# Optimization experiments

Hardware: AMD Instinct MI355X
Metric: run time of the kernel (lower is better)

The kernel has to match this reference:

```python
import jax, jax.numpy as jnp
import numpy as np

B, S, D, H = 2, 2048, 1024, 16
DK = D // H
ROPE_BASE = 10000.0


def setup_inputs() -> dict:
    key = jax.random.key(0)
    ks = jax.random.split(key, 6)
    x = jax.random.normal(ks[0], (B, S, D), dtype=jnp.float32)
    # causal mask, broadcastable to [B,H,S,S]; masked_fill where mask==0
    mask = jnp.tril(jnp.ones((S, S), dtype=bool))[None, None]
    position_ids = jnp.tile(jnp.arange(S, dtype=jnp.int32)[None, :], (B, 1))
    sc = 1.0 / np.sqrt(D)
    Wq = jax.random.normal(ks[1], (D, D), dtype=jnp.float32) * sc
    Wk = jax.random.normal(ks[2], (D, D), dtype=jnp.float32) * sc
    Wv = jax.random.normal(ks[3], (D, D), dtype=jnp.float32) * sc
    Wo = jax.random.normal(ks[4], (D, D), dtype=jnp.float32) * sc
    bo = jnp.zeros((D,), dtype=jnp.float32)
    return {"x": x, "mask": mask, "position_ids": position_ids,
            "Wq": Wq, "Wk": Wk, "Wv": Wv, "Wo": Wo, "bo": bo}


def _rotate_half(t):
    t1, t2 = t[..., : t.shape[-1] // 2], t[..., t.shape[-1] // 2:]
    return jnp.concatenate((-t2, t1), axis=-1)


def reference(x, mask, position_ids, Wq, Wk, Wv, Wo, bo):
    b, s, d = x.shape
    h, dk = H, DK
    scale = 1.0 / np.sqrt(dk)

    def proj(W):  # torch Linear: x @ W.T -> [b,h,s,dk]
        return (x @ W.T).reshape(b, s, h, dk).transpose(0, 2, 1, 3)

    Q, K, V = proj(Wq), proj(Wk), proj(Wv)

    # rotary tables (computed in fp32, matching RotaryEmbedding)
    inv_freq = 1.0 / (ROPE_BASE ** (jnp.arange(0, dk, 2, dtype=jnp.float32) / dk))
    t = jnp.arange(s, dtype=jnp.float32)
    freqs = jnp.outer(t, inv_freq)            # [s, dk/2]
    emb = jnp.concatenate((freqs, freqs), -1) # [s, dk]
    cos = jnp.cos(emb)[position_ids][:, None]  # [b,1,s,dk]
    sin = jnp.sin(emb)[position_ids][:, None]
    Q = Q * cos + _rotate_half(Q) * sin
    K = K * cos + _rotate_half(K) * sin

    scores = jnp.einsum('bhqd,bhkd->bhqk', Q, K) * scale
    scores = jnp.where(mask, scores, jnp.float32(-1e9))
    attn = jax.nn.softmax(scores, axis=-1)  # dropout is identity in eval
    out = jnp.einsum('bhqk,bhkd->bhqd', attn, V)
    out = out.transpose(0, 2, 1, 3).reshape(b, s, d)
    return out @ Wo.T + bo
```

## Files before the change

### kernel.cpp

```cpp
#include <hip/hip_runtime.h>
#include <hip/hip_bf16.h>
#include <cstdint>

#define BB 2
#define SS 2048
#define DD 1024
#define HH 16
#define DK 64
#define MROWS (BB*SS)
#define NQKV  (3*DD)

typedef __bf16 bf16x8 __attribute__((ext_vector_type(8)));
typedef float  f32x4  __attribute__((ext_vector_type(4)));
typedef float  f32x16 __attribute__((ext_vector_type(16)));
typedef unsigned u32x2 __attribute__((ext_vector_type(2)));

static __device__ __forceinline__ unsigned short f2bf(float f) {
    __bf16 h = (__bf16)f;
    return __builtin_bit_cast(unsigned short, h);
}
static __device__ __forceinline__ float bf2f(unsigned short u) {
    return (float)__builtin_bit_cast(__bf16, u);
}

#define GLOAD16(gsrc, ldst) \
    __builtin_amdgcn_global_load_lds((const __attribute__((address_space(1))) void*)(gsrc), \
                                     (__attribute__((address_space(3))) void*)(ldst), 16, 0, 0)

static __device__ __forceinline__ void pl32_swap(unsigned &x, unsigned &y) {
#if __has_builtin(__builtin_amdgcn_permlane32_swap)
    u32x2 r = __builtin_amdgcn_permlane32_swap(x, y, false, false);
    x = r[0]; y = r[1];
#else
    asm volatile("v_permlane32_swap_b32 %0, %1" : "+v"(x), "+v"(y));
#endif
}
static __device__ __forceinline__ float swap_half(float v, bool hi) {
    unsigned x = __builtin_bit_cast(unsigned, v), y = x;
    pl32_swap(x, y);
    return __builtin_bit_cast(float, hi ? x : y);
}
template<int BASE> static __device__ __forceinline__ bf16x8 cvt_chunk(const f32x16 &p) {
    unsigned x0, y0, x1, y1;
    asm("v_cvt_pk_bf16_f32 %0, %1, %2" : "=v"(x0) : "v"(p[BASE+0]), "v"(p[BASE+1]));
    asm("v_cvt_pk_bf16_f32 %0, %1, %2" : "=v"(y0) : "v"(p[BASE+4]), "v"(p[BASE+5]));
    asm("v_cvt_pk_bf16_f32 %0, %1, %2" : "=v"(x1) : "v"(p[BASE+2]), "v"(p[BASE+3]));
    asm("v_cvt_pk_bf16_f32 %0, %1, %2" : "=v"(y1) : "v"(p[BASE+6]), "v"(p[BASE+7]));
    pl32_swap(x0, y0);
    pl32_swap(x1, y1);
    union { unsigned u[4]; bf16x8 v; } r;
    r.u[0] = x0; r.u[1] = x1; r.u[2] = y0; r.u[3] = y1;
    return r.v;
}

__global__ void cast_all(const float* __restrict__ x,  const float* __restrict__ wq,
                         const float* __restrict__ wk, const float* __restrict__ wv,
                         const float* __restrict__ wo,
                         unsigned short* __restrict__ xb, unsigned short* __restrict__ wqkv,
                         unsigned short* __restrict__ wob)
{
    const int NX = MROWS * DD;
    const int NW = DD * DD;
    const int total = (NX + 4 * NW) / 8;
    for (int i = blockIdx.x * blockDim.x + threadIdx.x; i < total; i += gridDim.x * blockDim.x) {
        int base = i * 8;
        const float* src; unsigned short* dst; int off;
        if      (base < NX)          { src = x;  dst = xb;          off = base; }
        else if (base < NX + NW)     { src = wq; dst = wqkv;        off = base - NX; }
        else if (base < NX + 2*NW)   { src = wk; dst = wqkv + NW;   off = base - NX - NW; }
        else if (base < NX + 3*NW)   { src = wv; dst = wqkv + 2*NW; off = base - NX - 2*NW; }
        else                         { src = wo; dst = wob;         off = base - NX - 3*NW; }
        float4 a = *(const float4*)(src + off);
        float4 b = *(const float4*)(src + off + 4);
        union { unsigned short s[8]; uint4 v; } u;
        u.s[0] = f2bf(a.x); u.s[1] = f2bf(a.y); u.s[2] = f2bf(a.z); u.s[3] = f2bf(a.w);
        u.s[4] = f2bf(b.x); u.s[5] = f2bf(b.y); u.s[6] = f2bf(b.z); u.s[7] = f2bf(b.w);
        *(uint4*)(dst + off) = u.v;
    }
}

__global__ void rope_table(float* __restrict__ tabc, float* __restrict__ tabs)
{
    int i = blockIdx.x * blockDim.x + threadIdx.x;
    int s = i >> 5, d = i & 31;
    float inv = exp2f(-(float)d * (13.287712379549449f / 32.f));
    float ang = (float)s * inv;
    tabc[i] = cosf(ang);
    tabs[i] = sinf(ang);
}

__global__ __launch_bounds__(256) void gemm_qkv(
    const unsigned short* __restrict__ A, const unsigned short* __restrict__ Bm,
    const int* __restrict__ pids,
    const float* __restrict__ tabc, const float* __restrict__ tabs,
    unsigned short* __restrict__ Qb, unsigned short* __restrict__ Kb,
    unsigned short* __restrict__ Vr)
{
    __shared__ __align__(16) unsigned short sA[128 * 64];
    __shared__ __align__(16) unsigned short sB[128 * 64];
    const int tid = threadIdx.x;
    const int w = tid >> 6, l = tid & 63;
    const int wm = w >> 1, wn = w & 1;
    const int lr = l & 15, lg = l >> 4;
    const int swz = (blockIdx.x & 7) * 96 + (blockIdx.x >> 3);
    const int bx = swz % 24, by = swz / 24;
    const int mBase = by * 128, nBase = bx * 128;
    const int srow = tid >> 3;
    const int skof = (tid & 7) * 8;

    f32x4 acc[4][4] = {};

    for (int kt = 0; kt < DD; kt += 64) {
        __syncthreads();
        #pragma unroll
        for (int i = 0; i < 4; ++i) {
            const unsigned short* srcA = A + (size_t)(mBase + i*32 + srow) * DD + kt + skof;
            GLOAD16(srcA, &sA[i*2048 + w*512]);
            const unsigned short* srcB = Bm + (size_t)(nBase + i*32 + srow) * DD + kt + skof;
            GLOAD16(srcB, &sB[i*2048 + w*512]);
        }
        __syncthreads();
        #pragma unroll
        for (int kk = 0; kk < 2; ++kk) {
            bf16x8 af[4], bfv[4];
            #pragma unroll
            for (int mi = 0; mi < 4; ++mi)
                af[mi] = *(const bf16x8*)&sA[(wm*64 + mi*16 + lr)*64 + kk*32 + lg*8];
            #pragma unroll
            for (int ni = 0; ni < 4; ++ni)
                bfv[ni] = *(const bf16x8*)&sB[(wn*64 + ni*16 + lr)*64 + kk*32 + lg*8];
            #pragma unroll
            for (int mi = 0; mi < 4; ++mi)
                #pragma unroll
                for (int ni = 0; ni < 4; ++ni)
                    acc[mi][ni] = __builtin_amdgcn_mfma_f32_16x16x32_bf16(af[mi], bfv[ni], acc[mi][ni], 0, 0, 0);
        }
    }

    if (bx < 16) {
        const bool isQ = bx < 8;
        unsigned short* dst = isQ ? Qb : Kb;
        const float qsc = isQ ? 0.1803368801111244f : 1.0f;
        const int colbase = (bx & 7)*128 + wn*64;
        #pragma unroll
        for (int mi = 0; mi < 4; ++mi) {
            #pragma unroll
            for (int j = 0; j < 4; ++j) {
                int row = mBase + wm*64 + mi*16 + lg*4 + j;
                int pos = pids[row];
                #pragma unroll
                for (int ni = 0; ni < 2; ++ni) {
                    int d = ni*16 + lr;
                    float cc = tabc[pos*32 + d];
                    float sn = tabs[pos*32 + d];
                    float a  = acc[mi][ni][j];
                    float bb = acc[mi][ni+2][j];
                    dst[(size_t)row * DD + colbase + d]      = f2bf((a*cc - bb*sn) * qsc);
                    dst[(size_t)row * DD + colbase + d + 32] = f2bf((bb*cc + a*sn) * qsc);
                }
            }
        }
    } else {
        const int colbase = (bx - 16)*128 + wn*64;
        #pragma unroll
        for (int mi = 0; mi < 4; ++mi) {
            #pragma unroll
            for (int j = 0; j < 4; ++j) {
                int row = mBase + wm*64 + mi*16 + lg*4 + j;
                #pragma unroll
                for (int ni = 0; ni < 4; ++ni)
                    Vr[(size_t)row * DD + colbase + ni*16 + lr] = f2bf(acc[mi][ni][j]);
            }
        }
    }
}

__global__ __launch_bounds__(256) void gemm_bt(
    const unsigned short* __restrict__ A, const unsigned short* __restrict__ Bm,
    float* __restrict__ Cout, const float* __restrict__ bias,
    int M, int N, int K)
{
    __shared__ __align__(16) unsigned short sA[128 * 64];
    __shared__ __align__(16) unsigned short sB[128 * 64];
    const int tid = threadIdx.x;
    const int w = tid >> 6, l = tid & 63;
    const int wm = w >> 1, wn = w & 1;
    const int lr = l & 15, lg = l >> 4;
    const int nwg = gridDim.x;
    const int cpx = nwg >> 3;
    const int swz = (blockIdx.x & 7) * cpx + (blockIdx.x >> 3);
    const int nbx = N >> 7;
    const int bx = swz % nbx, by = swz / nbx;
    const int mBase = by * 128, nBase = bx * 128;
    const int srow = tid >> 3;
    const int skof = (tid & 7) * 8;

    f32x4 acc[4][4] = {};

    for (int kt = 0; kt < K; kt += 64) {
        __syncthreads();
        #pragma unroll
        for (int i = 0; i < 4; ++i) {
            const unsigned short* srcA = A + (size_t)(mBase + i*32 + srow) * K + kt + skof;
            GLOAD16(srcA, &sA[i*2048 + w*512]);
            const unsigned short* srcB = Bm + (size_t)(nBase + i*32 + srow) * K + kt + skof;
            GLOAD16(srcB, &sB[i*2048 + w*512]);
        }
        __syncthreads();
        #pragma unroll
        for (int kk = 0; kk < 2; ++kk) {
            bf16x8 af[4], bfv[4];
            #pragma unroll
            for (int mi = 0; mi < 4; ++mi)
                af[mi] = *(const bf16x8*)&sA[(wm*64 + mi*16 + lr)*64 + kk*32 + lg*8];
            #pragma unroll
            for (int ni = 0; ni < 4; ++ni)
                bfv[ni] = *(const bf16x8*)&sB[(wn*64 + ni*16 + lr)*64 + kk*32 + lg*8];
            #pragma unroll
            for (int mi = 0; mi < 4; ++mi)
                #pragma unroll
                for (int ni = 0; ni < 4; ++ni)
                    acc[mi][ni] = __builtin_amdgcn_mfma_f32_16x16x32_bf16(af[mi], bfv[ni], acc[mi][ni], 0, 0, 0);
        }
    }
    #pragma unroll
    for (int mi = 0; mi < 4; ++mi) {
        #pragma unroll
        for (int j = 0; j < 4; ++j) {
            int row = mBase + wm*64 + mi*16 + lg*4 + j;
            #pragma unroll
            for (int ni = 0; ni < 4; ++ni) {
                int col = nBase + wn*64 + ni*16 + lr;
                Cout[(size_t)row * N + col] = acc[mi][ni][j] + bias[col];
            }
        }
    }
}

__global__ __launch_bounds__(256) void v_transpose(
    const unsigned short* __restrict__ Vr, unsigned short* __restrict__ Vt)
{
    __shared__ __align__(16) unsigned short sT[64 * 64];
    const int bh = blockIdx.y;
    const int st = blockIdx.x;
    const int b = bh >> 4, h = bh & 15;
    const int tid = threadIdx.x;
    #pragma unroll
    for (int i = 0; i < 2; ++i) {
        int c = tid + i*256;
        int s = c >> 3, cb = c & 7;
        const unsigned short* src = Vr + (size_t)(b*SS + st*64 + s) * DD + h*64 + cb*8;
        uint4 v = *(const uint4*)src;
        *(uint4*)&sT[s*64 + ((cb ^ (s >> 3)) * 8)] = v;
    }
    __syncthreads();
    #pragma unroll
    for (int i = 0; i < 2; ++i) {
        int c = tid + i*256;
        int d = c >> 3, sb = c & 7;
        union { unsigned short u[8]; uint4 v; } o;
        #pragma unroll
        for (int e = 0; e < 8; ++e) {
            int s = sb*8 + e;
            o.u[e] = sT[s*64 + (((d >> 3) ^ (s >> 3)) * 8) + (d & 7)];
        }
        *(uint4*)(Vt + (size_t)(bh*64 + d) * SS + st*64 + sb*8) = o.v;
    }
}

__global__ __launch_bounds__(128, 2) void attn_fwd(
    const unsigned short* __restrict__ Qb,
    const unsigned short* __restrict__ Kb,
    const unsigned short* __restrict__ Vt,
    unsigned short* __restrict__ Ob)
{
    __shared__ __align__(16) unsigned short sK[2][64 * 64];
    __shared__ __align__(16) unsigned short sV[2][64 * 64];
    const int tid = threadIdx.x;
    const int w = tid >> 6, l = tid & 63;
    const int lq = l & 31;
    const int hi5 = l >> 5;
    const bool hb = hi5 != 0;

    const int xcd = blockIdx.x & 7;
    const int c   = blockIdx.x >> 3;
    const int g   = c >> 5;
    const int s_  = c & 31;
    const int qt  = (g & 1) ? (31 - s_) : s_;
    const int bh  = xcd * 4 + g;
    const int b = bh >> 4, h = bh & 15;

    const int srow2 = tid >> 3;
    const int skof  = (tid & 7) * 8;
    const int sksw  = skof ^ ((srow2 & 7) * 8);
    const int sw    = (lq & 7) * 8;
    const float THR = 12.0f;

    const unsigned kR = (unsigned)((b*SS + srow2) * DD + h*64 + sksw);
    const unsigned vR = (unsigned)((bh*64 + srow2) * SS + sksw);

    bf16x8 qf[4];
    {
        const unsigned short* qp = Qb + (size_t)(b*SS + qt*64 + w*32 + lq) * DD + h*64 + hi5*8;
        #pragma unroll
        for (int dkc = 0; dkc < 4; ++dkc)
            qf[dkc] = *(const bf16x8*)(qp + dkc*16);
    }
    const int q_lane = qt*64 + w*32 + lq;

    f32x16 o0 = {}, o1 = {};
    float mrow = -3.0e38f, lsum = 0.f;
    int cur = 0;

    #pragma unroll
    for (int i = 0; i < 4; ++i) {
        GLOAD16(Kb + kR + (unsigned)(i << 14), &sK[0][i*1024 + w*512]);
        GLOAD16(Vt + vR + (unsigned)(i << 15), &sV[0][i*1024 + w*512]);
    }

    for (int kt = 0; kt <= qt; ++kt) {
        __syncthreads();
        if (kt < qt) {
            unsigned ko = (unsigned)(kt + 1) << 16;
            unsigned vo = (unsigned)(kt + 1) << 6;
            #pragma unroll
            for (int i = 0; i < 4; ++i) {
                GLOAD16(Kb + kR + ko + (unsigned)(i << 14), &sK[cur^1][i*1024 + w*512]);
                GLOAD16(Vt + vR + vo + (unsigned)(i << 15), &sV[cur^1][i*1024 + w*512]);
            }
        }

        f32x16 p0 = {}, p1 = {};
        __builtin_amdgcn_s_setprio(1);
        #pragma unroll
        for (int dkc = 0; dkc < 4; ++dkc) {
            bf16x8 k0 = *(const bf16x8*)&sK[cur][lq*64 + ((dkc*16 + hi5*8) ^ sw)];
            p0 = __builtin_amdgcn_mfma_f32_32x32x16_bf16(k0, qf[dkc], p0, 0, 0, 0);
        }
        #pragma unroll
        for (int dkc = 0; dkc < 4; ++dkc) {
            bf16x8 k1 = *(const bf16x8*)&sK[cur][(32 + lq)*64 + ((dkc*16 + hi5*8) ^ sw)];
            p1 = __builtin_amdgcn_mfma_f32_32x32x16_bf16(k1, qf[dkc], p1, 0, 0, 0);
        }
        __builtin_amdgcn_s_setprio(0);

        if (kt == qt) {
            const int kb0 = kt*64 + 4*hi5;
            #pragma unroll
            for (int r = 0; r < 16; ++r) {
                const int cr = (r & 3) + 8*(r >> 2);
                if (kb0 + cr > q_lane)      p0[r] = -1e30f;
                if (kb0 + 32 + cr > q_lane) p1[r] = -1e30f;
            }
        }

        float tt[16];
        #pragma unroll
        for (int r = 0; r < 16; ++r) tt[r] = fmaxf(p0[r], p1[r]);
        #pragma unroll
        for (int s2 = 8; s2 >= 1; s2 >>= 1)
            #pragma unroll
            for (int r = 0; r < 8; ++r)
                if (r < s2) tt[r] = fmaxf(tt[r], tt[r + s2]);
        float tmx = fmaxf(tt[0], swap_half(tt[0], hb));

        float growth = tmx - mrow;
        if (!__all(growth <= THR)) {
            float mnew = fmaxf(mrow, tmx);
            float alpha = exp2f(mrow - mnew);
            lsum *= alpha;
            mrow = mnew;
            #pragma unroll
            for (int r = 0; r < 16; ++r) { o0[r] *= alpha; o1[r] *= alpha; }
        }

        #pragma unroll
        for (int r = 0; r < 16; ++r) {
            p0[r] = exp2f(p0[r] - mrow);
            p1[r] = exp2f(p1[r] - mrow);
        }
        float st[16];
        #pragma unroll
        for (int r = 0; r < 16; ++r) st[r] = p0[r] + p1[r];
        #pragma unroll
        for (int s2 = 8; s2 >= 1; s2 >>= 1)
            #pragma unroll
            for (int r = 0; r < 8; ++r)
                if (r < s2) st[r] += st[r + s2];
        lsum += st[0];

        __builtin_amdgcn_s_setprio(1);
        {
            bf16x8 pa, vf;
            pa = cvt_chunk<0>(p0);
            vf = *(const bf16x8*)&sV[cur][lq*64 + ((0*16 + hi5*8) ^ sw)];
            o0 = __builtin_amdgcn_mfma_f32_32x32x16_bf16(vf, pa, o0, 0, 0, 0);
            vf = *(const bf16x8*)&sV[cur][(32 + lq)*64 + ((0*16 + hi5*8) ^ sw)];
            o1 = __builtin_amdgcn_mfma_f32_32x32x16_bf16(vf, pa, o1, 0, 0, 0);
            pa = cvt_chunk<8>(p0);
            vf = *(const bf16x8*)&sV[cur][lq*64 + ((1*16 + hi5*8) ^ sw)];
            o0 = __builtin_amdgcn_mfma_f32_32x32x16_bf16(vf, pa, o0, 0, 0, 0);
            vf = *(const bf16x8*)&sV[cur][(32 + lq)*64 + ((1*16 + hi5*8) ^ sw)];
            o1 = __builtin_amdgcn_mfma_f32_32x32x16_bf16(vf, pa, o1, 0, 0, 0);
            pa = cvt_chunk<0>(p1);
            vf = *(const bf16x8*)&sV[cur][lq*64 + ((2*16 + hi5*8) ^ sw)];
            o0 = __builtin_amdgcn_mfma_f32_32x32x16_bf16(vf, pa, o0, 0, 0, 0);
            vf = *(const bf16x8*)&sV[cur][(32 + lq)*64 + ((2*16 + hi5*8) ^ sw)];
            o1 = __builtin_amdgcn_mfma_f32_32x32x16_bf16(vf, pa, o1, 0, 0, 0);
            pa = cvt_chunk<8>(p1);
            vf = *(const bf16x8*)&sV[cur][lq*64 + ((3*16 + hi5*8) ^ sw)];
            o0 = __builtin_amdgcn_mfma_f32_32x32x16_bf16(vf, pa, o0, 0, 0, 0);
            vf = *(const bf16x8*)&sV[cur][(32 + lq)*64 + ((3*16 + hi5*8) ^ sw)];
            o1 = __builtin_amdgcn_mfma_f32_32x32x16_bf16(vf, pa, o1, 0, 0, 0);
        }
        __builtin_amdgcn_s_setprio(0);
        cur ^= 1;
    }

    __syncthreads();
    float ls = lsum + swap_half(lsum, hb);
    float inv = 1.f / ls;
    unsigned short* sO = &sK[0][0] + w * 2048;

    #pragma unroll
    for (int g2 = 0; g2 < 4; ++g2) {
        unsigned ua, ub; uint2 t2;
        float v0 = o0[g2*4+0]*inv, v1 = o0[g2*4+1]*inv, v2 = o0[g2*4+2]*inv, v3 = o0[g2*4+3]*inv;
        asm("v_cvt_pk_bf16_f32 %0, %1, %2" : "=v"(ua) : "v"(v0), "v"(v1));
        asm("v_cvt_pk_bf16_f32 %0, %1, %2" : "=v"(ub) : "v"(v2), "v"(v3));
        t2.x = ua; t2.y = ub;
        *(uint2*)&sO[lq*64 + g2*8 + hi5*4] = t2;
        float w0 = o1[g2*4+0]*inv, w1 = o1[g2*4+1]*inv, w2 = o1[g2*4+2]*inv, w3 = o1[g2*4+3]*inv;
        asm("v_cvt_pk_bf16_f32 %0, %1, %2" : "=v"(ua) : "v"(w0), "v"(w1));
        asm("v_cvt_pk_bf16_f32 %0, %1, %2" : "=v"(ub) : "v"(w2), "v"(w3));
        t2.x = ua; t2.y = ub;
        *(uint2*)&sO[lq*64 + 32 + g2*8 + hi5*4] = t2;
    }
    asm volatile("s_waitcnt lgkmcnt(0)" ::: "memory");
    __builtin_amdgcn_sched_barrier(0);

    const int row = l >> 1, cb2 = (l & 1) * 32;
    const unsigned short* sOr = sO + row*64 + cb2;
    unsigned short* gp = Ob + (size_t)(b*SS + qt*64 + w*32 + row) * DD + h*64 + cb2;
    #pragma unroll
    for (int c2 = 0; c2 < 4; ++c2)
        *(uint4*)(gp + c2*8) = *(const uint4*)(sOr + c2*8);
}

extern "C" void kernel_launch(void* const* d_in, const int* in_sizes, int n_in,
                              void* d_out, int out_size, void* d_ws, size_t ws_size,
                              hipStream_t stream)
{
    const float* x  = (const float*)d_in[0];
    const int* pids = (const int*)d_in[2];
    const float* wq = (const float*)d_in[3];
    const float* wk = (const float*)d_in[4];
    const float* wv = (const float*)d_in[5];
    const float* wo = (const float*)d_in[6];
    const float* bo = (const float*)d_in[7];
    float* out = (float*)d_out;

    char* ws = (char*)d_ws;
    unsigned short* xb   = (unsigned short*)(ws);
    unsigned short* wqkv = (unsigned short*)(ws + (size_t)( 8u<<20));
    unsigned short* wob  = (unsigned short*)(ws + (size_t)(14u<<20));
    unsigned short* Vr   = (unsigned short*)(ws + (size_t)(16u<<20));
    unsigned short* Qb   = (unsigned short*)(ws + (size_t)(40u<<20));
    unsigned short* Kb   = (unsigned short*)(ws + (size_t)(48u<<20));
    unsigned short* Vt   = (unsigned short*)(ws + (size_t)(56u<<20));
    float* tabc          = (float*)(ws + (size_t)(64u<<20));
    float* tabs          = (float*)(ws + (size_t)(64u<<20) + (256u<<10));
    unsigned short* Ob   = xb;

    cast_all<<<dim3(4096), dim3(256), 0, stream>>>(x, wq, wk, wv, wo, xb, wqkv, wob);
    rope_table<<<dim3(256), dim3(256), 0, stream>>>(tabc, tabs);
    gemm_qkv<<<dim3(768), dim3(256), 0, stream>>>(
        xb, wqkv, pids, tabc, tabs, Qb, Kb, Vr);
    v_transpose<<<dim3(32, 32), dim3(256), 0, stream>>>(Vr, Vt);
    attn_fwd<<<dim3(1024), dim3(128), 0, stream>>>(Qb, Kb, Vt, Ob);
    gemm_bt<<<dim3(256), dim3(256), 0, stream>>>(
        Ob, wob, out, bo, MROWS, DD, DD);
}
```

Baseline: 151.5 us.

## Double-buffer shared memory tiles in QKV and output GEMMs

Both bf16 MFMA GEMM kernels now keep two shared-memory buffers for the A and B tiles. A prologue loads the first K-tile, and each iteration issues the next tile's global-to-LDS loads before computing on the current one. This removes one barrier per iteration and lets memory traffic overlap the MFMA work. In exchange, shared memory per block doubles to 64 KB, which can lower occupancy. Correctness relies on the barrier at the top of each iteration also waiting for the outstanding async loads.

```diff
diff --git a/kernel.cpp b/kernel.cpp
--- a/kernel.cpp
+++ b/kernel.cpp
@@ -96,8 +96,8 @@
     unsigned short* __restrict__ Qb, unsigned short* __restrict__ Kb,
     unsigned short* __restrict__ Vr)
 {
-    __shared__ __align__(16) unsigned short sA[128 * 64];
-    __shared__ __align__(16) unsigned short sB[128 * 64];
+    __shared__ __align__(16) unsigned short sA[2][128 * 64];
+    __shared__ __align__(16) unsigned short sB[2][128 * 64];
     const int tid = threadIdx.x;
     const int w = tid >> 6, l = tid & 63;
     const int wm = w >> 1, wn = w & 1;
@@ -110,31 +110,38 @@
 
     f32x4 acc[4][4] = {};
 
+    #pragma unroll
+    for (int i = 0; i < 4; ++i) {
+        GLOAD16(A  + (size_t)(mBase + i*32 + srow) * DD + skof, &sA[0][i*2048 + w*512]);
+        GLOAD16(Bm + (size_t)(nBase + i*32 + srow) * DD + skof, &sB[0][i*2048 + w*512]);
+    }
+    int cur = 0;
+
     for (int kt = 0; kt < DD; kt += 64) {
         __syncthreads();
-        #pragma unroll
-        for (int i = 0; i < 4; ++i) {
-            const unsigned short* srcA = A + (size_t)(mBase + i*32 + srow) * DD + kt + skof;
-            GLOAD16(srcA, &sA[i*2048 + w*512]);
-            const unsigned short* srcB = Bm + (size_t)(nBase + i*32 + srow) * DD + kt + skof;
-            GLOAD16(srcB, &sB[i*2048 + w*512]);
-        }
-        __syncthreads();
+        if (kt + 64 < DD) {
+            #pragma unroll
+            for (int i = 0; i < 4; ++i) {
+                GLOAD16(A  + (size_t)(mBase + i*32 + srow) * DD + kt + 64 + skof, &sA[cur^1][i*2048 + w*512]);
+                GLOAD16(Bm + (size_t)(nBase + i*32 + srow) * DD + kt + 64 + skof, &sB[cur^1][i*2048 + w*512]);
+            }
+        }
         #pragma unroll
         for (int kk = 0; kk < 2; ++kk) {
             bf16x8 af[4], bfv[4];
             #pragma unroll
             for (int mi = 0; mi < 4; ++mi)
-                af[mi] = *(const bf16x8*)&sA[(wm*64 + mi*16 + lr)*64 + kk*32 + lg*8];
+                af[mi] = *(const bf16x8*)&sA[cur][(wm*64 + mi*16 + lr)*64 + kk*32 + lg*8];
             #pragma unroll
             for (int ni = 0; ni < 4; ++ni)
-                bfv[ni] = *(const bf16x8*)&sB[(wn*64 + ni*16 + lr)*64 + kk*32 + lg*8];
+                bfv[ni] = *(const bf16x8*)&sB[cur][(wn*64 + ni*16 + lr)*64 + kk*32 + lg*8];
             #pragma unroll
             for (int mi = 0; mi < 4; ++mi)
                 #pragma unroll
                 for (int ni = 0; ni < 4; ++ni)
                     acc[mi][ni] = __builtin_amdgcn_mfma_f32_16x16x32_bf16(af[mi], bfv[ni], acc[mi][ni], 0, 0, 0);
         }
+        cur ^= 1;
     }
 
     if (bx < 16) {
@@ -180,8 +187,8 @@
     float* __restrict__ Cout, const float* __restrict__ bias,
     int M, int N, int K)
 {
-    __shared__ __align__(16) unsigned short sA[128 * 64];
-    __shared__ __align__(16) unsigned short sB[128 * 64];
+    __shared__ __align__(16) unsigned short sA[2][128 * 64];
+    __shared__ __align__(16) unsigned short sB[2][128 * 64];
     const int tid = threadIdx.x;
     const int w = tid >> 6, l = tid & 63;
     const int wm = w >> 1, wn = w & 1;
@@ -197,31 +204,38 @@
 
     f32x4 acc[4][4] = {};
 
+    #pragma unroll
+    for (int i = 0; i < 4; ++i) {
+        GLOAD16(A  + (size_t)(mBase + i*32 + srow) * K + skof, &sA[0][i*2048 + w*512]);
+        GLOAD16(Bm + (size_t)(nBase + i*32 + srow) * K + skof, &sB[0][i*2048 + w*512]);
+    }
+    int cur = 0;
+
     for (int kt = 0; kt < K; kt += 64) {
         __syncthreads();
-        #pragma unroll
-        for (int i = 0; i < 4; ++i) {
-            const unsigned short* srcA = A + (size_t)(mBase + i*32 + srow) * K + kt + skof;
-            GLOAD16(srcA, &sA[i*2048 + w*512]);
-            const unsigned short* srcB = Bm + (size_t)(nBase + i*32 + srow) * K + kt + skof;
-            GLOAD16(srcB, &sB[i*2048 + w*512]);
-        }
-        __syncthreads();
+        if (kt + 64 < K) {
+            #pragma unroll
+            for (int i = 0; i < 4; ++i) {
+                GLOAD16(A  + (size_t)(mBase + i*32 + srow) * K + kt + 64 + skof, &sA[cur^1][i*2048 + w*512]);
+                GLOAD16(Bm + (size_t)(nBase + i*32 + srow) * K + kt + 64 + skof, &sB[cur^1][i*2048 + w*512]);
+            }
+        }
         #pragma unroll
         for (int kk = 0; kk < 2; ++kk) {
             bf16x8 af[4], bfv[4];
             #pragma unroll
             for (int mi = 0; mi < 4; ++mi)
-                af[mi] = *(const bf16x8*)&sA[(wm*64 + mi*16 + lr)*64 + kk*32 + lg*8];
+                af[mi] = *(const bf16x8*)&sA[cur][(wm*64 + mi*16 + lr)*64 + kk*32 + lg*8];
             #pragma unroll
             for (int ni = 0; ni < 4; ++ni)
-                bfv[ni] = *(const bf16x8*)&sB[(wn*64 + ni*16 + lr)*64 + kk*32 + lg*8];
+                bfv[ni] = *(const bf16x8*)&sB[cur][(wn*64 + ni*16 + lr)*64 + kk*32 + lg*8];
             #pragma unroll
             for (int mi = 0; mi < 4; ++mi)
                 #pragma unroll
                 for (int ni = 0; ni < 4; ++ni)
                     acc[mi][ni] = __builtin_amdgcn_mfma_f32_16x16x32_bf16(af[mi], bfv[ni], acc[mi][ni], 0, 0, 0);
         }
+        cur ^= 1;
     }
     #pragma unroll
     for (int mi = 0; mi < 4; ++mi) {
```

New measurement: 147.4 us. -2.7%, faster.

## Share K/V tiles across four waves covering 128 query rows per block

Applied to the files above, without the earlier changes.

The attention kernel grows from 2 to 4 waves per block, so each block covers 128 query rows instead of 64 and each staged K/V tile is reused by twice as many queries. This halves the grid and the global-to-LDS K/V traffic per query. The block-to-tile mapping is redone to pair short and long causal tiles, and the causal mask is now tested per wave. In exchange, lower-row waves do some wasted work on fully masked tiles near the diagonal, and fewer, larger blocks may balance less evenly across CUs.

```diff
diff --git a/kernel.cpp b/kernel.cpp
--- a/kernel.cpp
+++ b/kernel.cpp
@@ -268,7 +268,7 @@
     }
 }
 
-__global__ __launch_bounds__(128, 2) void attn_fwd(
+__global__ __launch_bounds__(256, 2) void attn_fwd(
     const unsigned short* __restrict__ Qb,
     const unsigned short* __restrict__ Kb,
     const unsigned short* __restrict__ Vt,
@@ -282,52 +282,54 @@
     const int hi5 = l >> 5;
     const bool hb = hi5 != 0;
 
-    const int xcd = blockIdx.x & 7;
-    const int c   = blockIdx.x >> 3;
-    const int g   = c >> 5;
-    const int s_  = c & 31;
-    const int qt  = (g & 1) ? (31 - s_) : s_;
-    const int bh  = xcd * 4 + g;
+    const int xcd  = blockIdx.x & 7;
+    const int c    = blockIdx.x >> 3;
+    const int gsel = c & 3;
+    const int t    = c >> 2;
+    const int qt   = (t < 8) ? t : 23 - t;
+    const int bh   = xcd * 4 + gsel;
     const int b = bh >> 4, h = bh & 15;
 
-    const int srow2 = tid >> 3;
-    const int skof  = (tid & 7) * 8;
-    const int sksw  = skof ^ ((srow2 & 7) * 8);
-    const int sw    = (lq & 7) * 8;
+    const int srow = tid >> 3;
+    const int skof = (tid & 7) * 8;
+    const int sksw = skof ^ ((srow & 7) * 8);
+    const int sw   = (lq & 7) * 8;
     const float THR = 12.0f;
 
-    const unsigned kR = (unsigned)((b*SS + srow2) * DD + h*64 + sksw);
-    const unsigned vR = (unsigned)((bh*64 + srow2) * SS + sksw);
+    const unsigned kR0 = (unsigned)((b*SS + srow) * DD + h*64 + sksw);
+    const unsigned kR1 = kR0 + (unsigned)(32 * DD);
+    const unsigned vR0 = (unsigned)((bh*64 + srow) * SS + sksw);
+    const unsigned vR1 = vR0 + (unsigned)(32 * SS);
 
     bf16x8 qf[4];
     {
-        const unsigned short* qp = Qb + (size_t)(b*SS + qt*64 + w*32 + lq) * DD + h*64 + hi5*8;
+        const unsigned short* qp = Qb + (size_t)(b*SS + qt*128 + w*32 + lq) * DD + h*64 + hi5*8;
         #pragma unroll
         for (int dkc = 0; dkc < 4; ++dkc)
             qf[dkc] = *(const bf16x8*)(qp + dkc*16);
     }
-    const int q_lane = qt*64 + w*32 + lq;
+    const int q_lane = qt*128 + w*32 + lq;
+    const int wbase  = qt*128 + w*32;
+    const int total  = 2*qt + 2;
 
     f32x16 o0 = {}, o1 = {};
     float mrow = -3.0e38f, lsum = 0.f;
     int cur = 0;
 
-    #pragma unroll
-    for (int i = 0; i < 4; ++i) {
-        GLOAD16(Kb + kR + (unsigned)(i << 14), &sK[0][i*1024 + w*512]);
-        GLOAD16(Vt + vR + (unsigned)(i << 15), &sV[0][i*1024 + w*512]);
-    }
-
-    for (int kt = 0; kt <= qt; ++kt) {
+    GLOAD16(Kb + kR0, &sK[0][w*512]);
+    GLOAD16(Kb + kR1, &sK[0][2048 + w*512]);
+    GLOAD16(Vt + vR0, &sV[0][w*512]);
+    GLOAD16(Vt + vR1, &sV[0][2048 + w*512]);
+
+    for (int kt = 0; kt < total; ++kt) {
         __syncthreads();
-        if (kt < qt) {
+        if (kt + 1 < total) {
             unsigned ko = (unsigned)(kt + 1) << 16;
             unsigned vo = (unsigned)(kt + 1) << 6;
-            #pragma unroll
-            for (int i = 0; i < 4; ++i) {
-                GLOAD16(Kb + kR + ko + (unsigned)(i << 14), &sK[cur^1][i*1024 + w*512]);
-                GLOAD16(Vt + vR + vo + (unsigned)(i << 15), &sV[cur^1][i*1024 + w*512]);
-            }
+            GLOAD16(Kb + kR0 + ko, &sK[cur^1][w*512]);
+            GLOAD16(Kb + kR1 + ko, &sK[cur^1][2048 + w*512]);
+            GLOAD16(Vt + vR0 + vo, &sV[cur^1][w*512]);
+            GLOAD16(Vt + vR1 + vo, &sV[cur^1][2048 + w*512]);
         }
 
         f32x16 p0 = {}, p1 = {};
@@ -344,7 +346,7 @@
         }
         __builtin_amdgcn_s_setprio(0);
 
-        if (kt == qt) {
+        if (kt*64 + 63 > wbase) {
             const int kb0 = kt*64 + 4*hi5;
             #pragma unroll
             for (int r = 0; r < 16; ++r) {
@@ -441,7 +443,7 @@
 
     const int row = l >> 1, cb2 = (l & 1) * 32;
     const unsigned short* sOr = sO + row*64 + cb2;
-    unsigned short* gp = Ob + (size_t)(b*SS + qt*64 + w*32 + row) * DD + h*64 + cb2;
+    unsigned short* gp = Ob + (size_t)(b*SS + qt*128 + w*32 + row) * DD + h*64 + cb2;
     #pragma unroll
     for (int c2 = 0; c2 < 4; ++c2)
         *(uint4*)(gp + c2*8) = *(const uint4*)(sOr + c2*8);
@@ -477,7 +479,7 @@
     gemm_qkv<<<dim3(768), dim3(256), 0, stream>>>(
         xb, wqkv, pids, tabc, tabs, Qb, Kb, Vr);
     v_transpose<<<dim3(32, 32), dim3(256), 0, stream>>>(Vr, Vt);
-    attn_fwd<<<dim3(1024), dim3(128), 0, stream>>>(Qb, Kb, Vt, Ob);
+    attn_fwd<<<dim3(512), dim3(256), 0, stream>>>(Qb, Kb, Vt, Ob);
     gemm_bt<<<dim3(256), dim3(256), 0, stream>>>(
         Ob, wob, out, bo, MROWS, DD, DD);
 }
```

New measurement: 151.3 us. No clear change (-0.2%).
